# Kernel tuning notes

Hardware: AMD Instinct MI355X
Metric: run time of the kernel (lower is better)

Reference implementation:

```python
import jax, jax.numpy as jnp
import numpy as np

BETA = 10.0  # fixed buffer: torch.ones(1, num_centers) * 10


def setup_inputs() -> dict:
    key = jax.random.key(0)
    k1, k2, k3 = jax.random.split(key, 3)
    n, M, d, n_out = 65536, 1024, 64, 3
    x = jax.random.normal(k1, (n, d), dtype=jnp.float32)
    centers = jax.random.normal(k2, (M, d), dtype=jnp.float32)
    # nn.Linear init in the module: weight ~ N(0, 0.02), bias = 0
    W = jax.random.normal(k3, (n_out, M + d), dtype=jnp.float32) * 0.02
    b = jnp.zeros((n_out,), dtype=jnp.float32)
    return {"x": x, "centers": centers, "W": W, "b": b}


def reference(x, centers, W, b):
    x2 = jnp.sum(x * x, axis=1, keepdims=True)          # [n, 1]
    c2 = jnp.sum(centers * centers, axis=1)             # [M]
    d2 = x2 + c2[None, :] - 2.0 * (x @ centers.T)       # [n, M]
    rbf = jnp.exp(-BETA * d2)                           # Gaussian RBF
    feat = jnp.concatenate([x, rbf], axis=1)            # [n, d + M]
    return feat @ W.T + b                               # [n, n_out]
```

## Files before the change

kernel.cpp:

```cpp
#include <hip/hip_runtime.h>
#include <hip/hip_bf16.h>
#include <math.h>

typedef short bf16x8 __attribute__((ext_vector_type(8)));
typedef float f32x4 __attribute__((ext_vector_type(4)));
typedef unsigned int uint32;

#define BETA 10.0f
#define PRUNE_THRESH -80.0f

__device__ __forceinline__ uint32 f2bf_rtne(float f) {
    uint32 u = __float_as_uint(f);
    u += 0x7FFFu + ((u >> 16) & 1u);
    return u >> 16;
}
__device__ __forceinline__ uint32 pk_rtne(float a, float b) {
    return f2bf_rtne(a) | (f2bf_rtne(b) << 16);
}
__device__ __forceinline__ uint32 pk_trunc(float a, float b) {
    return (__float_as_uint(a) >> 16) | (__float_as_uint(b) & 0xFFFF0000u);
}
__device__ __forceinline__ f32x4 vmax4(f32x4 a, f32x4 b) {
    f32x4 r;
    r[0] = fmaxf(a[0], b[0]); r[1] = fmaxf(a[1], b[1]);
    r[2] = fmaxf(a[2], b[2]); r[3] = fmaxf(a[3], b[3]);
    return r;
}

#define GLDS(g, l) __builtin_amdgcn_global_load_lds( \
    (const __attribute__((address_space(1))) unsigned int*)(g), \
    (__attribute__((address_space(3))) unsigned int*)(l), 16, 0, 0)

__global__ void rbfn_prep(const float* __restrict__ centers,
                          uint32* __restrict__ cbf,
                          float* __restrict__ c2m) {
    const int tid = threadIdx.x;
    const int j = blockIdx.x * 64 + (tid >> 2);
    const int seg = tid & 3;
    const float4* cp = (const float4*)(centers + j * 64 + seg * 16);
    const float4 f0 = cp[0], f1 = cp[1], f2 = cp[2], f3 = cp[3];
    float s = f0.x*f0.x + f0.y*f0.y + f0.z*f0.z + f0.w*f0.w
            + f1.x*f1.x + f1.y*f1.y + f1.z*f1.z + f1.w*f1.w
            + f2.x*f2.x + f2.y*f2.y + f2.z*f2.z + f2.w*f2.w
            + f3.x*f3.x + f3.y*f3.y + f3.z*f3.z + f3.w*f3.w;
    uint4 p0, p1;
    p0.x = pk_rtne(f0.x, f0.y); p0.y = pk_rtne(f0.z, f0.w);
    p0.z = pk_rtne(f1.x, f1.y); p0.w = pk_rtne(f1.z, f1.w);
    p1.x = pk_rtne(f2.x, f2.y); p1.y = pk_rtne(f2.z, f2.w);
    p1.z = pk_rtne(f3.x, f3.y); p1.w = pk_rtne(f3.z, f3.w);
    const int c0 = seg * 2, c1 = seg * 2 + 1;
    char* base = (char*)cbf + j * 128;
    *(uint4*)(base + (((c0 + j) & 7) << 4)) = p0;
    *(uint4*)(base + (((c1 + j) & 7) << 4)) = p1;
    s += __shfl_xor(s, 1);
    s += __shfl_xor(s, 2);
    if (seg == 0) c2m[j] = -BETA * s;
}

struct AccPack { f32x4 a[8]; };

__device__ __attribute__((noinline)) void rbfn_slow(
    AccPack ap, float* red, const float* x2p, const float* W,
    float c2ct, int j, int rbase, int quad) {
    #pragma unroll
    for (int rt = 0; rt < 8; ++rt) {
        #pragma unroll
        for (int rg = 0; rg < 4; ++rg) {
            const int r = rbase + rt * 16 + quad * 4 + rg;
            const float arg = fmaf(2.0f * BETA, ap.a[rt][rg], c2ct - BETA * x2p[r]);
            if (arg > PRUNE_THRESH) {
                const float e = expf(arg);
                atomicAdd(&red[r * 3 + 0], e * W[0 * 1088 + 64 + j]);
                atomicAdd(&red[r * 3 + 1], e * W[1 * 1088 + 64 + j]);
                atomicAdd(&red[r * 3 + 2], e * W[2 * 1088 + 64 + j]);
            }
        }
    }
}

__global__ __launch_bounds__(512, 2) void rbfn_main(
    const float* __restrict__ x,
    const uint32* __restrict__ cbf,
    const float* __restrict__ c2m,
    const float* __restrict__ W,
    const float* __restrict__ bias,
    float* __restrict__ out)
{
    __shared__ __align__(16) char  lds_cbf[131072];
    __shared__ __align__(16) float lds_x2[256];
    __shared__ __align__(16) float red[768];

    const int tid = threadIdx.x;
    const int wv = tid >> 6;
    const int lane = tid & 63;
    const int quad = lane >> 4;
    const int l15 = lane & 15;
    const int rowgrp = wv >> 2;
    const int colgrp = wv & 3;
    const int row0 = blockIdx.x * 256;

    {
        const char* g = (const char*)cbf + wv * 1024 + lane * 16;
        char* l = lds_cbf + wv * 1024;
        #pragma unroll
        for (int it = 0; it < 16; ++it)
            GLDS(g + it * 8192, l + it * 8192);
    }

    const int seg = tid & 15;
    const float4 w0 = *(const float4*)(W + 0 * 1088 + seg * 4);
    const float4 w1 = *(const float4*)(W + 1 * 1088 + seg * 4);
    const float4 w2 = *(const float4*)(W + 2 * 1088 + seg * 4);

    const float4* x4 = (const float4*)x;
    #pragma unroll
    for (int p = 0; p < 8; ++p) {
        const int chunk = p * 512 + tid;
        const float4 v = x4[(size_t)row0 * 16 + chunk];
        float s2 = v.x * v.x + v.y * v.y + v.z * v.z + v.w * v.w;
        float d0 = v.x * w0.x + v.y * w0.y + v.z * w0.z + v.w * w0.w;
        float d1 = v.x * w1.x + v.y * w1.y + v.z * w1.z + v.w * w1.w;
        float d2 = v.x * w2.x + v.y * w2.y + v.z * w2.z + v.w * w2.w;
        #pragma unroll
        for (int m = 1; m <= 8; m <<= 1) {
            s2 += __shfl_xor(s2, m);
            d0 += __shfl_xor(d0, m);
            d1 += __shfl_xor(d1, m);
            d2 += __shfl_xor(d2, m);
        }
        if (seg == 0) {
            const int r = chunk >> 4;
            lds_x2[r] = s2;
            red[r * 3 + 0] = d0;
            red[r * 3 + 1] = d1;
            red[r * 3 + 2] = d2;
        }
    }

    bf16x8 af[8][2];
    #pragma unroll
    for (int rt = 0; rt < 8; ++rt) {
        const float4* px = (const float4*)(x + (size_t)(row0 + rowgrp * 128 + rt * 16 + l15) * 64) + quad * 2;
        #pragma unroll
        for (int kk = 0; kk < 2; ++kk) {
            const float4 u0 = px[kk * 8];
            const float4 u1 = px[kk * 8 + 1];
            union { bf16x8 v; uint4 u; } t;
            t.u.x = pk_trunc(u0.x, u0.y);
            t.u.y = pk_trunc(u0.z, u0.w);
            t.u.z = pk_trunc(u1.x, u1.y);
            t.u.w = pk_trunc(u1.z, u1.w);
            af[rt][kk] = t.v;
        }
    }

    float c2r[16];
    const int jb = colgrp * 256 + l15;
    #pragma unroll
    for (int ct = 0; ct < 16; ++ct)
        c2r[ct] = c2m[jb + ct * 16];

    __syncthreads();

    float mn = 1e30f;
    #pragma unroll
    for (int rt = 0; rt < 8; ++rt) {
        const float4 q = *(const float4*)&lds_x2[rowgrp * 128 + rt * 16 + quad * 4];
        mn = fminf(mn, fminf(fminf(q.x, q.y), fminf(q.z, q.w)));
    }
    const float pm = -BETA * mn;

    const char* cb = lds_cbf;
    const int base0 = jb * 128 + (((quad + jb) & 7) << 4);
    const int base1 = jb * 128 + (((quad + 4 + jb) & 7) << 4);
    bf16x8 b0 = *(const bf16x8*)(cb + base0);
    bf16x8 b1 = *(const bf16x8*)(cb + base1);
    #pragma unroll
    for (int ct = 0; ct < 16; ++ct) {
        bf16x8 nb0 = b0, nb1 = b1;
        if (ct < 15) {
            nb0 = *(const bf16x8*)(cb + base0 + (ct + 1) * 2048);
            nb1 = *(const bf16x8*)(cb + base1 + (ct + 1) * 2048);
        }
        f32x4 acc[8];
        #pragma unroll
        for (int rt = 0; rt < 8; ++rt) {
            const f32x4 z = {0.f, 0.f, 0.f, 0.f};
            acc[rt] = __builtin_amdgcn_mfma_f32_16x16x32_bf16(af[rt][0], b0, z, 0, 0, 0);
            acc[rt] = __builtin_amdgcn_mfma_f32_16x16x32_bf16(af[rt][1], b1, acc[rt], 0, 0, 0);
        }
        f32x4 m0 = vmax4(acc[0], acc[1]);
        f32x4 m1 = vmax4(acc[2], acc[3]);
        f32x4 m2 = vmax4(acc[4], acc[5]);
        f32x4 m3 = vmax4(acc[6], acc[7]);
        m0 = vmax4(m0, m1);
        m2 = vmax4(m2, m3);
        m0 = vmax4(m0, m2);
        const float mx = fmaxf(fmaxf(m0[0], m0[1]), fmaxf(m0[2], m0[3]));
        const float bound = fmaf(2.0f * BETA, mx, pm + c2r[ct]);
        if (__builtin_expect(__ballot(bound > PRUNE_THRESH) != 0ull, 0)) {
            AccPack ap;
            #pragma unroll
            for (int rt = 0; rt < 8; ++rt) ap.a[rt] = acc[rt];
            rbfn_slow(ap, red, lds_x2, W, c2r[ct], jb + ct * 16, rowgrp * 128, quad);
        }
        b0 = nb0; b1 = nb1;
    }

    __syncthreads();

    if (tid < 192) {
        const float4 rv = *((const float4*)red + tid);
        float4 o;
        o.x = rv.x + bias[(tid + 0) % 3];
        o.y = rv.y + bias[(tid + 1) % 3];
        o.z = rv.z + bias[(tid + 2) % 3];
        o.w = rv.w + bias[(tid + 3) % 3];
        ((float4*)out)[blockIdx.x * 192 + tid] = o;
    }
}

extern "C" void kernel_launch(void* const* d_in, const int* in_sizes, int n_in,
                              void* d_out, int out_size, void* d_ws, size_t ws_size,
                              hipStream_t stream) {
    const float* x       = (const float*)d_in[0];
    const float* centers = (const float*)d_in[1];
    const float* W       = (const float*)d_in[2];
    const float* b       = (const float*)d_in[3];
    float* out = (float*)d_out;

    float*  c2m = (float*)d_ws;
    uint32* cbf = (uint32*)((char*)d_ws + 4096);

    const int n = in_sizes[0] / 64;

    rbfn_prep<<<16, 256, 0, stream>>>(centers, cbf, c2m);
    rbfn_main<<<n / 256, 512, 0, stream>>>(x, cbf, c2m, W, b, out);
}
```

Baseline: 87.65 us.

## Split center columns across two blocks and recompute rare survivors in exact fp32

Each block now handles 128 rows and half of the 1024 centers, so it needs half the LDS (64KB) and can run at higher occupancy (launch bounds 4). Partial outputs from the two blocks are combined with global atomics into a zero-initialised output, with a memset added before launch. The pruning check becomes a per-row exact max of the exponent argument, taken across the whole column tile and tested once after the loop. The rare slow path recomputes distances in fp32 straight from the centers instead of reusing the bf16 accumulators. The costs are an extra memset, global atomics, and a very slow scalar fallback if pruning ever fails.

```diff
diff --git a/kernel.cpp b/kernel.cpp
--- a/kernel.cpp
+++ b/kernel.cpp
@@ -7,7 +7,7 @@
 typedef unsigned int uint32;
 
 #define BETA 10.0f
-#define PRUNE_THRESH -80.0f
+#define THRESH -80.0f
 
 __device__ __forceinline__ uint32 f2bf_rtne(float f) {
     uint32 u = __float_as_uint(f);
@@ -19,12 +19,6 @@
 }
 __device__ __forceinline__ uint32 pk_trunc(float a, float b) {
     return (__float_as_uint(a) >> 16) | (__float_as_uint(b) & 0xFFFF0000u);
-}
-__device__ __forceinline__ f32x4 vmax4(f32x4 a, f32x4 b) {
-    f32x4 r;
-    r[0] = fmaxf(a[0], b[0]); r[1] = fmaxf(a[1], b[1]);
-    r[2] = fmaxf(a[2], b[2]); r[3] = fmaxf(a[3], b[3]);
-    return r;
 }
 
 #define GLDS(g, l) __builtin_amdgcn_global_load_lds( \
@@ -57,38 +51,19 @@
     if (seg == 0) c2m[j] = -BETA * s;
 }
 
-struct AccPack { f32x4 a[8]; };
-
-__device__ __attribute__((noinline)) void rbfn_slow(
-    AccPack ap, float* red, const float* x2p, const float* W,
-    float c2ct, int j, int rbase, int quad) {
-    #pragma unroll
-    for (int rt = 0; rt < 8; ++rt) {
-        #pragma unroll
-        for (int rg = 0; rg < 4; ++rg) {
-            const int r = rbase + rt * 16 + quad * 4 + rg;
-            const float arg = fmaf(2.0f * BETA, ap.a[rt][rg], c2ct - BETA * x2p[r]);
-            if (arg > PRUNE_THRESH) {
-                const float e = expf(arg);
-                atomicAdd(&red[r * 3 + 0], e * W[0 * 1088 + 64 + j]);
-                atomicAdd(&red[r * 3 + 1], e * W[1 * 1088 + 64 + j]);
-                atomicAdd(&red[r * 3 + 2], e * W[2 * 1088 + 64 + j]);
-            }
-        }
-    }
-}
-
-__global__ __launch_bounds__(512, 2) void rbfn_main(
+__global__ __launch_bounds__(512, 4) void rbfn_main(
     const float* __restrict__ x,
     const uint32* __restrict__ cbf,
     const float* __restrict__ c2m,
     const float* __restrict__ W,
     const float* __restrict__ bias,
+    const float* __restrict__ centers,
     float* __restrict__ out)
 {
-    __shared__ __align__(16) char  lds_cbf[131072];
-    __shared__ __align__(16) float lds_x2[256];
-    __shared__ __align__(16) float red[768];
+    __shared__ __align__(16) char   lds_cbf[65536];
+    __shared__ __align__(16) float4 scratch[4][128];
+    __shared__ __align__(16) float  lds_x2[128];
+    __shared__ __align__(16) float  red[384];
 
     const int tid = threadIdx.x;
     const int wv = tid >> 6;
@@ -97,50 +72,47 @@
     const int l15 = lane & 15;
     const int rowgrp = wv >> 2;
     const int colgrp = wv & 3;
-    const int row0 = blockIdx.x * 256;
+    const int ch = blockIdx.x & 1;
+    const int rb = blockIdx.x >> 1;
+    const int row0 = rb * 128;
+    const int col0 = ch * 512;
 
     {
-        const char* g = (const char*)cbf + wv * 1024 + lane * 16;
+        const char* g = (const char*)cbf + col0 * 128 + wv * 1024 + lane * 16;
         char* l = lds_cbf + wv * 1024;
         #pragma unroll
-        for (int it = 0; it < 16; ++it)
+        for (int it = 0; it < 8; ++it)
             GLDS(g + it * 8192, l + it * 8192);
     }
 
-    const int seg = tid & 15;
-    const float4 w0 = *(const float4*)(W + 0 * 1088 + seg * 4);
-    const float4 w1 = *(const float4*)(W + 1 * 1088 + seg * 4);
-    const float4 w2 = *(const float4*)(W + 2 * 1088 + seg * 4);
-
-    const float4* x4 = (const float4*)x;
-    #pragma unroll
-    for (int p = 0; p < 8; ++p) {
-        const int chunk = p * 512 + tid;
-        const float4 v = x4[(size_t)row0 * 16 + chunk];
-        float s2 = v.x * v.x + v.y * v.y + v.z * v.z + v.w * v.w;
-        float d0 = v.x * w0.x + v.y * w0.y + v.z * w0.z + v.w * w0.w;
-        float d1 = v.x * w1.x + v.y * w1.y + v.z * w1.z + v.w * w1.w;
-        float d2 = v.x * w2.x + v.y * w2.y + v.z * w2.z + v.w * w2.w;
-        #pragma unroll
-        for (int m = 1; m <= 8; m <<= 1) {
-            s2 += __shfl_xor(s2, m);
-            d0 += __shfl_xor(d0, m);
-            d1 += __shfl_xor(d1, m);
-            d2 += __shfl_xor(d2, m);
-        }
-        if (seg == 0) {
-            const int r = chunk >> 4;
-            lds_x2[r] = s2;
-            red[r * 3 + 0] = d0;
-            red[r * 3 + 1] = d1;
-            red[r * 3 + 2] = d2;
-        }
-    }
-
-    bf16x8 af[8][2];
-    #pragma unroll
-    for (int rt = 0; rt < 8; ++rt) {
-        const float4* px = (const float4*)(x + (size_t)(row0 + rowgrp * 128 + rt * 16 + l15) * 64) + quad * 2;
+    {
+        const int r = tid & 127, q = tid >> 7;
+        const float4* px = (const float4*)(x + (size_t)(row0 + r) * 64) + q * 4;
+        const float4 v0 = px[0], v1 = px[1], v2 = px[2], v3 = px[3];
+        const float4* w0p = (const float4*)(W + 0 * 1088 + q * 16);
+        const float4* w1p = (const float4*)(W + 1 * 1088 + q * 16);
+        const float4* w2p = (const float4*)(W + 2 * 1088 + q * 16);
+        float s2 = v0.x*v0.x + v0.y*v0.y + v0.z*v0.z + v0.w*v0.w
+                 + v1.x*v1.x + v1.y*v1.y + v1.z*v1.z + v1.w*v1.w
+                 + v2.x*v2.x + v2.y*v2.y + v2.z*v2.z + v2.w*v2.w
+                 + v3.x*v3.x + v3.y*v3.y + v3.z*v3.z + v3.w*v3.w;
+        float d0 = 0.f, d1 = 0.f, d2 = 0.f;
+        const float4 vv[4] = {v0, v1, v2, v3};
+        #pragma unroll
+        for (int i = 0; i < 4; ++i) {
+            const float4 a = vv[i], b0 = w0p[i], b1 = w1p[i], b2 = w2p[i];
+            d0 += a.x*b0.x + a.y*b0.y + a.z*b0.z + a.w*b0.w;
+            d1 += a.x*b1.x + a.y*b1.y + a.z*b1.z + a.w*b1.w;
+            d2 += a.x*b2.x + a.y*b2.y + a.z*b2.z + a.w*b2.w;
+        }
+        float4 o; o.x = s2; o.y = d0; o.z = d1; o.w = d2;
+        scratch[q][r] = o;
+    }
+
+    bf16x8 af[4][2];
+    #pragma unroll
+    for (int rt = 0; rt < 4; ++rt) {
+        const float4* px = (const float4*)(x + (size_t)(row0 + rowgrp * 64 + rt * 16 + l15) * 64) + quad * 2;
         #pragma unroll
         for (int kk = 0; kk < 2; ++kk) {
             const float4 u0 = px[kk * 8];
@@ -154,70 +126,94 @@
         }
     }
 
-    float c2r[16];
-    const int jb = colgrp * 256 + l15;
-    #pragma unroll
-    for (int ct = 0; ct < 16; ++ct)
-        c2r[ct] = c2m[jb + ct * 16];
+    float c2r[8];
+    #pragma unroll
+    for (int ct = 0; ct < 8; ++ct)
+        c2r[ct] = c2m[col0 + colgrp * 128 + ct * 16 + l15];
 
     __syncthreads();
 
-    float mn = 1e30f;
-    #pragma unroll
-    for (int rt = 0; rt < 8; ++rt) {
-        const float4 q = *(const float4*)&lds_x2[rowgrp * 128 + rt * 16 + quad * 4];
-        mn = fminf(mn, fminf(fminf(q.x, q.y), fminf(q.z, q.w)));
-    }
-    const float pm = -BETA * mn;
+    if (tid < 128) {
+        const float4 a = scratch[0][tid], b = scratch[1][tid];
+        const float4 c = scratch[2][tid], d = scratch[3][tid];
+        lds_x2[tid] = a.x + b.x + c.x + d.x;
+        const float z = (ch == 0) ? 1.f : 0.f;
+        red[tid * 3 + 0] = (a.y + b.y + c.y + d.y + bias[0]) * z;
+        red[tid * 3 + 1] = (a.z + b.z + c.z + d.z + bias[1]) * z;
+        red[tid * 3 + 2] = (a.w + b.w + c.w + d.w + bias[2]) * z;
+    }
+    __syncthreads();
+
+    float prer[16];
+    #pragma unroll
+    for (int rt = 0; rt < 4; ++rt) {
+        const float4 q4 = *(const float4*)&lds_x2[rowgrp * 64 + rt * 16 + quad * 4];
+        prer[rt * 4 + 0] = -BETA * q4.x;
+        prer[rt * 4 + 1] = -BETA * q4.y;
+        prer[rt * 4 + 2] = -BETA * q4.z;
+        prer[rt * 4 + 3] = -BETA * q4.w;
+    }
 
     const char* cb = lds_cbf;
-    const int base0 = jb * 128 + (((quad + jb) & 7) << 4);
-    const int base1 = jb * 128 + (((quad + 4 + jb) & 7) << 4);
+    const int jl = colgrp * 128 + l15;
+    const int base0 = jl * 128 + (((quad + jl) & 7) << 4);
+    const int base1 = jl * 128 + (((quad + 4 + jl) & 7) << 4);
     bf16x8 b0 = *(const bf16x8*)(cb + base0);
     bf16x8 b1 = *(const bf16x8*)(cb + base1);
-    #pragma unroll
-    for (int ct = 0; ct < 16; ++ct) {
+    float gmax = -1e30f;
+    #pragma unroll
+    for (int ct = 0; ct < 8; ++ct) {
         bf16x8 nb0 = b0, nb1 = b1;
-        if (ct < 15) {
+        if (ct < 7) {
             nb0 = *(const bf16x8*)(cb + base0 + (ct + 1) * 2048);
             nb1 = *(const bf16x8*)(cb + base1 + (ct + 1) * 2048);
         }
-        f32x4 acc[8];
-        #pragma unroll
-        for (int rt = 0; rt < 8; ++rt) {
+        f32x4 acc[4];
+        #pragma unroll
+        for (int rt = 0; rt < 4; ++rt) {
             const f32x4 z = {0.f, 0.f, 0.f, 0.f};
             acc[rt] = __builtin_amdgcn_mfma_f32_16x16x32_bf16(af[rt][0], b0, z, 0, 0, 0);
             acc[rt] = __builtin_amdgcn_mfma_f32_16x16x32_bf16(af[rt][1], b1, acc[rt], 0, 0, 0);
         }
-        f32x4 m0 = vmax4(acc[0], acc[1]);
-        f32x4 m1 = vmax4(acc[2], acc[3]);
-        f32x4 m2 = vmax4(acc[4], acc[5]);
-        f32x4 m3 = vmax4(acc[6], acc[7]);
-        m0 = vmax4(m0, m1);
-        m2 = vmax4(m2, m3);
-        m0 = vmax4(m0, m2);
-        const float mx = fmaxf(fmaxf(m0[0], m0[1]), fmaxf(m0[2], m0[3]));
-        const float bound = fmaf(2.0f * BETA, mx, pm + c2r[ct]);
-        if (__builtin_expect(__ballot(bound > PRUNE_THRESH) != 0ull, 0)) {
-            AccPack ap;
+        float m = -1e30f;
+        #pragma unroll
+        for (int rt = 0; rt < 4; ++rt)
             #pragma unroll
-            for (int rt = 0; rt < 8; ++rt) ap.a[rt] = acc[rt];
-            rbfn_slow(ap, red, lds_x2, W, c2r[ct], jb + ct * 16, rowgrp * 128, quad);
-        }
+            for (int rg = 0; rg < 4; ++rg)
+                m = fmaxf(m, fmaf(acc[rt][rg], 2.0f * BETA, prer[rt * 4 + rg]));
+        gmax = fmaxf(gmax, m + c2r[ct]);
         b0 = nb0; b1 = nb1;
     }
 
+    if (__builtin_expect(__ballot(gmax > THRESH) != 0ull, 0)) {
+        #pragma clang loop unroll(disable)
+        for (int ct = 0; ct < 8; ++ct) {
+            const int j = col0 + colgrp * 128 + ct * 16 + l15;
+            #pragma clang loop unroll(disable)
+            for (int rr = 0; rr < 16; ++rr) {
+                const int r = rowgrp * 64 + (rr >> 2) * 16 + quad * 4 + (rr & 3);
+                const float* xr = x + (size_t)(row0 + r) * 64;
+                const float* cr = centers + (size_t)j * 64;
+                float d2 = 0.f;
+                #pragma clang loop unroll(disable)
+                for (int k = 0; k < 64; ++k) {
+                    const float df = xr[k] - cr[k];
+                    d2 = fmaf(df, df, d2);
+                }
+                const float arg = -BETA * d2;
+                if (arg > -87.f) {
+                    const float e = expf(arg);
+                    atomicAdd(&red[r * 3 + 0], e * W[0 * 1088 + 64 + j]);
+                    atomicAdd(&red[r * 3 + 1], e * W[1 * 1088 + 64 + j]);
+                    atomicAdd(&red[r * 3 + 2], e * W[2 * 1088 + 64 + j]);
+                }
+            }
+        }
+    }
     __syncthreads();
 
-    if (tid < 192) {
-        const float4 rv = *((const float4*)red + tid);
-        float4 o;
-        o.x = rv.x + bias[(tid + 0) % 3];
-        o.y = rv.y + bias[(tid + 1) % 3];
-        o.z = rv.z + bias[(tid + 2) % 3];
-        o.w = rv.w + bias[(tid + 3) % 3];
-        ((float4*)out)[blockIdx.x * 192 + tid] = o;
-    }
+    if (tid < 384)
+        atomicAdd(out + (size_t)row0 * 3 + tid, red[tid]);
 }
 
 extern "C" void kernel_launch(void* const* d_in, const int* in_sizes, int n_in,
@@ -234,6 +230,7 @@
 
     const int n = in_sizes[0] / 64;
 
+    hipMemsetAsync(d_out, 0, (size_t)out_size * sizeof(float), stream);
     rbfn_prep<<<16, 256, 0, stream>>>(centers, cbf, c2m);
-    rbfn_main<<<n / 256, 512, 0, stream>>>(x, cbf, c2m, W, b, out);
-}
+    rbfn_main<<<(n / 128) * 2, 512, 0, stream>>>(x, cbf, c2m, W, b, centers, out);
+}
```

Measured after the change: 96.58 us. +10.2%, slower.
